# Optimization experiments

Hardware: AMD Instinct MI355X
Metric: run time of the kernel (lower is better)

The kernel has to match this reference:

```python
import jax, jax.numpy as jnp
import numpy as np

B, T, C, NH = 8, 1024, 768, 12
HD = C // NH


def setup_inputs() -> dict:
    key = jax.random.key(0)
    k1, k2, k3, k4, k5 = jax.random.split(key, 5)
    s = 0.02
    return {
        "x": jax.random.normal(k1, (B, T, C), dtype=jnp.float32),
        "w_attn": jax.random.normal(k2, (C, 3 * C), dtype=jnp.float32) * s,
        "b_attn": jax.random.normal(k3, (3 * C,), dtype=jnp.float32) * s,
        "w_proj": jax.random.normal(k4, (C, C), dtype=jnp.float32) * s,
        "b_proj": jax.random.normal(k5, (C,), dtype=jnp.float32) * s,
    }


def reference(x, w_attn, b_attn, w_proj, b_proj):
    Bv, Tv, Cv = x.shape
    # fused QKV projection
    qkv = jnp.einsum('btc,cd->btd', x, w_attn) + b_attn  # [B,T,3C]
    q, k, v = jnp.split(qkv, 3, axis=-1)
    # [B, NH, T, HD]
    q = q.reshape(Bv, Tv, NH, HD).transpose(0, 2, 1, 3)
    k = k.reshape(Bv, Tv, NH, HD).transpose(0, 2, 1, 3)
    v = v.reshape(Bv, Tv, NH, HD).transpose(0, 2, 1, 3)
    scale = 1.0 / np.sqrt(HD).astype(np.float32)
    att = jnp.einsum('bhqd,bhkd->bhqk', q, k) * scale  # [B,NH,T,T]
    causal = jnp.tril(jnp.ones((Tv, Tv), dtype=bool))
    att = jnp.where(causal, att, -jnp.inf)
    att = jax.nn.softmax(att, axis=-1)
    y = jnp.einsum('bhqk,bhkd->bhqd', att, v)  # [B,NH,T,HD]
    y = y.transpose(0, 2, 1, 3).reshape(Bv, Tv, Cv)
    return jnp.einsum('btc,cd->btd', y, w_proj) + b_proj
```

## Files before the change

kernel.cpp:

```cpp
#include <hip/hip_runtime.h>

constexpr int kB  = 8;
constexpr int kT  = 1024;
constexpr int kC  = 768;
constexpr int kNH = 12;
constexpr int kHD = 64;
constexpr int kM  = kB * kT;
constexpr int k3C = 3 * kC;

using bf16x8 = __attribute__((ext_vector_type(8))) __bf16;
using f32x4  = __attribute__((ext_vector_type(4))) float;

__device__ __forceinline__ float bf2f(unsigned short u) {
    union { unsigned int i; float f; } v;
    v.i = ((unsigned int)u) << 16;
    return v.f;
}

__device__ __forceinline__ unsigned short f2bf(float f) {
    union { float f; unsigned int u; } v; v.f = f;
    unsigned int r = v.u + 0x7fffu + ((v.u >> 16) & 1u);
    return (unsigned short)(r >> 16);
}

__device__ __forceinline__ void async16(const void* g, void* l) {
    __builtin_amdgcn_global_load_lds(
        (__attribute__((address_space(1))) void*)g,
        (__attribute__((address_space(3))) void*)l, 16, 0, 0);
}

__device__ __forceinline__ void wait_vm0() {
    __builtin_amdgcn_s_waitcnt(0x0F70);
}


__global__ __launch_bounds__(256) void cvt_bf16_kernel(
    const float* __restrict__ in, unsigned short* __restrict__ out)
{
    const int i = blockIdx.x * 256 + threadIdx.x;
    const float4 v = ((const float4*)in)[i];
    ushort4 o;
    o.x = f2bf(v.x); o.y = f2bf(v.y); o.z = f2bf(v.z); o.w = f2bf(v.w);
    ((ushort4*)out)[i] = o;
}

__global__ __launch_bounds__(256) void transpose_cvt_kernel(
    const float* __restrict__ W, unsigned short* __restrict__ Wt, int K, int N)
{
    __shared__ float tile[32][33];
    const int tx = threadIdx.x & 31, ty = threadIdx.x >> 5;
    const int n0 = blockIdx.x * 32, k0 = blockIdx.y * 32;
    #pragma unroll
    for (int i = 0; i < 4; ++i)
        tile[ty + i * 8][tx] = W[(size_t)(k0 + ty + i * 8) * N + n0 + tx];
    __syncthreads();
    #pragma unroll
    for (int i = 0; i < 4; ++i)
        Wt[(size_t)(n0 + ty + i * 8) * K + k0 + tx] = f2bf(tile[tx][ty + i * 8]);
}

__global__ __launch_bounds__(256) void vtrans_kernel(
    const unsigned short* __restrict__ qkv, unsigned short* __restrict__ VT)
{
    __shared__ unsigned short tile[64][72];
    const int tid = threadIdx.x;
    const int bh = blockIdx.x >> 4;
    const int b = bh / kNH, h = bh % kNH;
    const int tt = (blockIdx.x & 15) * 64;
    const int row = tid >> 2;
    const int c0  = (tid & 3) * 16;
    const unsigned short* src =
        qkv + (size_t)(b * kT + tt + row) * k3C + 2 * kC + h * kHD + c0;
    *(uint4*)&tile[row][c0]     = *(const uint4*)src;
    *(uint4*)&tile[row][c0 + 8] = *(const uint4*)(src + 8);
    __syncthreads();
    const int d  = tid >> 2;
    const int t8 = (tid & 3) * 16;
    unsigned short tmp[16];
    #pragma unroll
    for (int i = 0; i < 16; ++i) tmp[i] = tile[t8 + i][d];
    unsigned short* dst = VT + ((size_t)bh * kHD + d) * kT + tt + t8;
    *(uint4*)dst       = *(uint4*)&tmp[0];
    *(uint4*)(dst + 8) = *(uint4*)&tmp[8];
}

template<int NSUB, bool OUT_BF16>
__global__ __launch_bounds__(256) void gemm_mfma_kernel(
    const unsigned short* __restrict__ A, int lda,
    const unsigned short* __restrict__ Bt,
    const float* __restrict__ bias,
    void* __restrict__ outv, int N, int K)
{
    constexpr int NW = NSUB / 2;
    constexpr int BB = NSUB / 4;
    alignas(16) __shared__ unsigned short As[2][8 * 512];
    alignas(16) __shared__ unsigned short Bs[2][NSUB * 512];

    const int tid  = threadIdx.x;
    const int w    = tid >> 6;
    const int lane = tid & 63;
    const int wr = w >> 1, wc = w & 1;
    const int m0 = blockIdx.y * 128, n0 = blockIdx.x * (NSUB * 16);

    const int fr = lane & 15;
    const int fk = (lane >> 4) * 8;

    auto stage = [&](int bufi, int kt) {
        #pragma unroll
        for (int t = 0; t < 2; ++t) {
            const int fa = w * 2 + t;
            const unsigned short* ga =
                A + (size_t)(m0 + fa * 16 + fr) * lda + kt + fk;
            async16(ga, &As[bufi][fa * 512]);
        }
        #pragma unroll
        for (int t = 0; t < BB; ++t) {
            const int fb = w * BB + t;
            const unsigned short* gb =
                Bt + (size_t)(n0 + fb * 16 + fr) * K + kt + fk;
            async16(gb, &Bs[bufi][fb * 512]);
        }
    };

    f32x4 acc[4][NW];
    #pragma unroll
    for (int i = 0; i < 4; ++i)
        #pragma unroll
        for (int j = 0; j < NW; ++j) {
            f32x4 z = {0.f, 0.f, 0.f, 0.f};
            acc[i][j] = z;
        }

    stage(0, 0);
    const int niter = K / 32;
    for (int it = 0; it < niter; ++it) {
        const int buf = it & 1;
        wait_vm0();
        __syncthreads();
        if (it + 1 < niter) stage(1 - buf, (it + 1) * 32);

        bf16x8 a[4], b[NW];
        #pragma unroll
        for (int i = 0; i < 4; ++i)
            a[i] = *(const bf16x8*)&As[buf][(wr * 4 + i) * 512 + lane * 8];
        #pragma unroll
        for (int j = 0; j < NW; ++j)
            b[j] = *(const bf16x8*)&Bs[buf][(wc * NW + j) * 512 + lane * 8];
        #pragma unroll
        for (int i = 0; i < 4; ++i)
            #pragma unroll
            for (int j = 0; j < NW; ++j)
                acc[i][j] = __builtin_amdgcn_mfma_f32_16x16x32_bf16(
                    a[i], b[j], acc[i][j], 0, 0, 0);
    }

    const int quad  = lane >> 4;
    const int col16 = lane & 15;
    float biasv[NW];
    #pragma unroll
    for (int j = 0; j < NW; ++j)
        biasv[j] = bias[n0 + wc * (NW * 16) + j * 16 + col16];

    #pragma unroll
    for (int i = 0; i < 4; ++i) {
        #pragma unroll
        for (int r = 0; r < 4; ++r) {
            const int row = m0 + wr * 64 + i * 16 + quad * 4 + r;
            #pragma unroll
            for (int j = 0; j < NW; ++j) {
                const int col = n0 + wc * (NW * 16) + j * 16 + col16;
                const float v = acc[i][j][r] + biasv[j];
                if (OUT_BF16)
                    ((unsigned short*)outv)[(size_t)row * N + col] = f2bf(v);
                else
                    ((float*)outv)[(size_t)row * N + col] = v;
            }
        }
    }
}

__global__ __launch_bounds__(256) void attn_mfma_kernel(
    const unsigned short* __restrict__ qkv,
    const unsigned short* __restrict__ VT,
    unsigned short* __restrict__ y)
{
    alignas(16) __shared__ unsigned short Kf[2][8 * 512];
    alignas(16) __shared__ unsigned short Vf[2][8 * 512];
    alignas(16) __shared__ unsigned short Pf[8 * 512];

    const int tid  = threadIdx.x;
    const int w    = tid >> 6;
    const int lane = tid & 63;
    const int quad = lane >> 4, l15 = lane & 15;
    const int bh  = blockIdx.x >> 3;
    const int b   = bh / kNH, h = bh % kNH;
    const int pid = blockIdx.x & 7;

    auto stage = [&](int bufi, int kbase) {
        const unsigned short* gk = qkv +
            (size_t)(b * kT + kbase + w * 16 + l15) * k3C + kC + h * kHD + quad * 8;
        async16(gk,      &Kf[bufi][(w * 2 + 0) * 512]);
        async16(gk + 32, &Kf[bufi][(w * 2 + 1) * 512]);
        const unsigned short* gv = VT +
            ((size_t)bh * kHD + w * 16 + l15) * kT + kbase + quad * 8;
        async16(gv,      &Vf[bufi][(w * 2 + 0) * 512]);
        async16(gv + 32, &Vf[bufi][(w * 2 + 1) * 512]);
    };

    #pragma unroll 1
    for (int phase = 0; phase < 2; ++phase) {
        const int t0 = (phase == 0 ? (15 - pid) : pid) * 64;
        const int nchunks = t0 / 64 + 1;

        __syncthreads();
        stage(0, 0);
        {
            const unsigned short* g0 = qkv +
                (size_t)(b * kT + t0 + w * 16 + l15) * k3C + h * kHD + quad * 8;
            async16(g0,      &Pf[(w * 2 + 0) * 512]);
            async16(g0 + 32, &Pf[(w * 2 + 1) * 512]);
        }
        wait_vm0();
        const bf16x8 aq0 = *(const bf16x8*)&Pf[(w * 2 + 0) * 512 + lane * 8];
        const bf16x8 aq1 = *(const bf16x8*)&Pf[(w * 2 + 1) * 512 + lane * 8];

        float m_run[4], l_run[4];
        f32x4 acc_o[4];
        #pragma unroll
        for (int r = 0; r < 4; ++r) { m_run[r] = -INFINITY; l_run[r] = 0.f; }
        #pragma unroll
        for (int n = 0; n < 4; ++n) {
            f32x4 z = {0.f, 0.f, 0.f, 0.f};
            acc_o[n] = z;
        }

        for (int c = 0; c < nchunks; ++c) {
            const int kbase = c * 64;
            const int buf = c & 1;
            wait_vm0();
            __syncthreads();
            if (c + 1 < nchunks) stage(1 - buf, kbase + 64);

            f32x4 acc_s[4];
            #pragma unroll
            for (int k = 0; k < 4; ++k) {
                f32x4 z = {0.f, 0.f, 0.f, 0.f};
                acc_s[k] = z;
            }
            #pragma unroll
            for (int ksub = 0; ksub < 4; ++ksub) {
                const bf16x8 bk0 =
                    *(const bf16x8*)&Kf[buf][(ksub * 2 + 0) * 512 + lane * 8];
                const bf16x8 bk1 =
                    *(const bf16x8*)&Kf[buf][(ksub * 2 + 1) * 512 + lane * 8];
                acc_s[ksub] = __builtin_amdgcn_mfma_f32_16x16x32_bf16(
                    aq0, bk0, acc_s[ksub], 0, 0, 0);
                acc_s[ksub] = __builtin_amdgcn_mfma_f32_16x16x32_bf16(
                    aq1, bk1, acc_s[ksub], 0, 0, 0);
            }

            float sv[4][4];
            #pragma unroll
            for (int ksub = 0; ksub < 4; ++ksub)
                #pragma unroll
                for (int r = 0; r < 4; ++r)
                    sv[ksub][r] = acc_s[ksub][r] * 0.125f;
            if (kbase == t0) {
                const int qrow = t0 + w * 16 + quad * 4;
                #pragma unroll
                for (int ksub = 0; ksub < 4; ++ksub) {
                    const int key = kbase + ksub * 16 + l15;
                    #pragma unroll
                    for (int r = 0; r < 4; ++r)
                        if (key > qrow + r) sv[ksub][r] = -INFINITY;
                }
            }

            float alpha[4];
            #pragma unroll
            for (int r = 0; r < 4; ++r) {
                float mx = fmaxf(fmaxf(sv[0][r], sv[1][r]),
                                 fmaxf(sv[2][r], sv[3][r]));
                mx = fmaxf(mx, __shfl_xor(mx, 1));
                mx = fmaxf(mx, __shfl_xor(mx, 2));
                mx = fmaxf(mx, __shfl_xor(mx, 4));
                mx = fmaxf(mx, __shfl_xor(mx, 8));
                const float m_new = fmaxf(m_run[r], mx);
                alpha[r] = __expf(m_run[r] - m_new);
                float ps = 0.f;
                #pragma unroll
                for (int ksub = 0; ksub < 4; ++ksub) {
                    sv[ksub][r] = __expf(sv[ksub][r] - m_new);
                    ps += sv[ksub][r];
                }
                ps += __shfl_xor(ps, 1);
                ps += __shfl_xor(ps, 2);
                ps += __shfl_xor(ps, 4);
                ps += __shfl_xor(ps, 8);
                l_run[r] = l_run[r] * alpha[r] + ps;
                m_run[r] = m_new;
            }

            #pragma unroll
            for (int ksub = 0; ksub < 4; ++ksub) {
                const int key = ksub * 16 + l15;
                #pragma unroll
                for (int r = 0; r < 4; ++r) {
                    const int lp = quad * 4 + r + ((key & 31) >> 3) * 16;
                    Pf[(w * 2 + (key >> 5)) * 512 + lp * 8 + (key & 7)] =
                        f2bf(sv[ksub][r]);
                }
            }

            #pragma unroll
            for (int n = 0; n < 4; ++n)
                #pragma unroll
                for (int r = 0; r < 4; ++r)
                    acc_o[n][r] *= alpha[r];
            const bf16x8 ap0 = *(const bf16x8*)&Pf[(w * 2 + 0) * 512 + lane * 8];
            const bf16x8 ap1 = *(const bf16x8*)&Pf[(w * 2 + 1) * 512 + lane * 8];
            #pragma unroll
            for (int nsub = 0; nsub < 4; ++nsub) {
                const bf16x8 bv0 =
                    *(const bf16x8*)&Vf[buf][(nsub * 2 + 0) * 512 + lane * 8];
                const bf16x8 bv1 =
                    *(const bf16x8*)&Vf[buf][(nsub * 2 + 1) * 512 + lane * 8];
                acc_o[nsub] = __builtin_amdgcn_mfma_f32_16x16x32_bf16(
                    ap0, bv0, acc_o[nsub], 0, 0, 0);
                acc_o[nsub] = __builtin_amdgcn_mfma_f32_16x16x32_bf16(
                    ap1, bv1, acc_o[nsub], 0, 0, 0);
            }
        }

        float inv[4];
        #pragma unroll
        for (int r = 0; r < 4; ++r) inv[r] = 1.0f / l_run[r];
        #pragma unroll
        for (int nsub = 0; nsub < 4; ++nsub)
            #pragma unroll
            for (int r = 0; r < 4; ++r)
                y[(size_t)(b * kT + t0 + w * 16 + quad * 4 + r) * kC +
                  h * kHD + nsub * 16 + l15] = f2bf(acc_o[nsub][r] * inv[r]);
    }
}

extern "C" void kernel_launch(void* const* d_in, const int* in_sizes, int n_in,
                              void* d_out, int out_size, void* d_ws, size_t ws_size,
                              hipStream_t stream) {
    const float* x      = (const float*)d_in[0];
    const float* w_attn = (const float*)d_in[1];
    const float* b_attn = (const float*)d_in[2];
    const float* w_proj = (const float*)d_in[3];
    const float* b_proj = (const float*)d_in[4];
    float* out = (float*)d_out;

    unsigned short* xb     = (unsigned short*)d_ws;
    unsigned short* VT     = xb;
    unsigned short* wattnT = xb     + (size_t)kM * kC;
    unsigned short* wprojT = wattnT + (size_t)k3C * kC;
    unsigned short* qkv    = wprojT + (size_t)kC * kC;
    unsigned short* yb     = qkv    + (size_t)kM * k3C;

    cvt_bf16_kernel<<<(kM * kC) / (4 * 256), 256, 0, stream>>>(x, xb);
    transpose_cvt_kernel<<<dim3(k3C / 32, kC / 32), 256, 0, stream>>>(
        w_attn, wattnT, kC, k3C);
    transpose_cvt_kernel<<<dim3(kC / 32, kC / 32), 256, 0, stream>>>(
        w_proj, wprojT, kC, kC);

    gemm_mfma_kernel<8, true><<<dim3(k3C / 128, kM / 128), 256, 0, stream>>>(
        xb, kC, wattnT, b_attn, qkv, k3C, kC);

    vtrans_kernel<<<kB * kNH * (kT / 64), 256, 0, stream>>>(qkv, VT);

    attn_mfma_kernel<<<kB * kNH * 8, 256, 0, stream>>>(qkv, VT, yb);

    gemm_mfma_kernel<4, false><<<dim3(kC / 64, kM / 128), 256, 0, stream>>>(
        yb, kC, wprojT, b_proj, out, kC, kC);
}
```

Before: 242.8 us.

## Fuse V transpose into QKV GEMM epilogue and triple-buffer GEMM loads

The QKV GEMM epilogue now writes the V columns straight into the transposed per-head VT layout, using 4-element vector stores along t. Q and K go to a compact 2C-wide buffer, so the separate V-transpose kernel and its round trip through global memory are removed. The GEMM main loop moves from double to triple buffering with a partial vmcnt wait and a raw s_barrier, keeping two tiles of loads in flight. Risks are correctness of the vmcnt count against outstanding loads, and whether the raw barrier still orders LDS reads before a buffer is overwritten.

```diff
diff --git a/kernel.cpp b/kernel.cpp
--- a/kernel.cpp
+++ b/kernel.cpp
@@ -7,15 +7,10 @@
 constexpr int kHD = 64;
 constexpr int kM  = kB * kT;
 constexpr int k3C = 3 * kC;
+constexpr int kQK = 2 * kC;
 
 using bf16x8 = __attribute__((ext_vector_type(8))) __bf16;
 using f32x4  = __attribute__((ext_vector_type(4))) float;
-
-__device__ __forceinline__ float bf2f(unsigned short u) {
-    union { unsigned int i; float f; } v;
-    v.i = ((unsigned int)u) << 16;
-    return v.f;
-}
 
 __device__ __forceinline__ unsigned short f2bf(float f) {
     union { float f; unsigned int u; } v; v.f = f;
@@ -29,9 +24,10 @@
         (__attribute__((address_space(3))) void*)l, 16, 0, 0);
 }
 
-__device__ __forceinline__ void wait_vm0() {
-    __builtin_amdgcn_s_waitcnt(0x0F70);
-}
+template<int IMM> __device__ __forceinline__ void wait_vm() {
+    __builtin_amdgcn_s_waitcnt(IMM);
+}
+__device__ __forceinline__ void wait_vm0() { __builtin_amdgcn_s_waitcnt(0x0F70); }
 
 
 __global__ __launch_bounds__(256) void cvt_bf16_kernel(
@@ -59,42 +55,22 @@
         Wt[(size_t)(n0 + ty + i * 8) * K + k0 + tx] = f2bf(tile[tx][ty + i * 8]);
 }
 
-__global__ __launch_bounds__(256) void vtrans_kernel(
-    const unsigned short* __restrict__ qkv, unsigned short* __restrict__ VT)
-{
-    __shared__ unsigned short tile[64][72];
-    const int tid = threadIdx.x;
-    const int bh = blockIdx.x >> 4;
-    const int b = bh / kNH, h = bh % kNH;
-    const int tt = (blockIdx.x & 15) * 64;
-    const int row = tid >> 2;
-    const int c0  = (tid & 3) * 16;
-    const unsigned short* src =
-        qkv + (size_t)(b * kT + tt + row) * k3C + 2 * kC + h * kHD + c0;
-    *(uint4*)&tile[row][c0]     = *(const uint4*)src;
-    *(uint4*)&tile[row][c0 + 8] = *(const uint4*)(src + 8);
-    __syncthreads();
-    const int d  = tid >> 2;
-    const int t8 = (tid & 3) * 16;
-    unsigned short tmp[16];
-    #pragma unroll
-    for (int i = 0; i < 16; ++i) tmp[i] = tile[t8 + i][d];
-    unsigned short* dst = VT + ((size_t)bh * kHD + d) * kT + tt + t8;
-    *(uint4*)dst       = *(uint4*)&tmp[0];
-    *(uint4*)(dst + 8) = *(uint4*)&tmp[8];
-}
-
-template<int NSUB, bool OUT_BF16>
+template<int NSUB, int MODE>
 __global__ __launch_bounds__(256) void gemm_mfma_kernel(
     const unsigned short* __restrict__ A, int lda,
     const unsigned short* __restrict__ Bt,
     const float* __restrict__ bias,
-    void* __restrict__ outv, int N, int K)
+    void* __restrict__ outv,
+    unsigned short* __restrict__ vt,
+    int N, int K)
 {
     constexpr int NW = NSUB / 2;
-    constexpr int BB = NSUB / 4;
-    alignas(16) __shared__ unsigned short As[2][8 * 512];
-    alignas(16) __shared__ unsigned short Bs[2][NSUB * 512];
+    constexpr int BB = (NSUB / 4 > 0) ? NSUB / 4 : 1;
+    constexpr int P  = 2 + BB;
+    constexpr int WAIT_P = 0x0F70 | P;
+
+    alignas(16) __shared__ unsigned short As[3][8 * 512];
+    alignas(16) __shared__ unsigned short Bs[3][NSUB * 512];
 
     const int tid  = threadIdx.x;
     const int w    = tid >> 6;
@@ -131,27 +107,32 @@
             acc[i][j] = z;
         }
 
+    const int niter = K / 32;
     stage(0, 0);
-    const int niter = K / 32;
+    stage(1, 32);
+    int cur = 0, pf = 2;
     for (int it = 0; it < niter; ++it) {
-        const int buf = it & 1;
-        wait_vm0();
-        __syncthreads();
-        if (it + 1 < niter) stage(1 - buf, (it + 1) * 32);
+        if (it + 1 < niter) wait_vm<WAIT_P>();
+        else               wait_vm<0x0F70>();
+        __builtin_amdgcn_s_barrier();
+        if (it + 2 < niter) stage(pf, (it + 2) * 32);
 
         bf16x8 a[4], b[NW];
         #pragma unroll
         for (int i = 0; i < 4; ++i)
-            a[i] = *(const bf16x8*)&As[buf][(wr * 4 + i) * 512 + lane * 8];
+            a[i] = *(const bf16x8*)&As[cur][(wr * 4 + i) * 512 + lane * 8];
         #pragma unroll
         for (int j = 0; j < NW; ++j)
-            b[j] = *(const bf16x8*)&Bs[buf][(wc * NW + j) * 512 + lane * 8];
+            b[j] = *(const bf16x8*)&Bs[cur][(wc * NW + j) * 512 + lane * 8];
         #pragma unroll
         for (int i = 0; i < 4; ++i)
             #pragma unroll
             for (int j = 0; j < NW; ++j)
                 acc[i][j] = __builtin_amdgcn_mfma_f32_16x16x32_bf16(
                     a[i], b[j], acc[i][j], 0, 0, 0);
+
+        cur = (cur == 2) ? 0 : cur + 1;
+        pf  = (pf  == 2) ? 0 : pf  + 1;
     }
 
     const int quad  = lane >> 4;
@@ -161,26 +142,46 @@
     for (int j = 0; j < NW; ++j)
         biasv[j] = bias[n0 + wc * (NW * 16) + j * 16 + col16];
 
-    #pragma unroll
-    for (int i = 0; i < 4; ++i) {
-        #pragma unroll
-        for (int r = 0; r < 4; ++r) {
-            const int row = m0 + wr * 64 + i * 16 + quad * 4 + r;
+    if (MODE == 1 && n0 >= kQK) {
+        const int bidx = m0 >> 10;
+        #pragma unroll
+        for (int i = 0; i < 4; ++i) {
+            const int row = m0 + wr * 64 + i * 16 + quad * 4;
+            const int t = row & 1023;
             #pragma unroll
             for (int j = 0; j < NW; ++j) {
-                const int col = n0 + wc * (NW * 16) + j * 16 + col16;
-                const float v = acc[i][j][r] + biasv[j];
-                if (OUT_BF16)
-                    ((unsigned short*)outv)[(size_t)row * N + col] = f2bf(v);
-                else
-                    ((float*)outv)[(size_t)row * N + col] = v;
+                const int hv = n0 + wc * (NW * 16) + j * 16 + col16 - kQK;
+                const int h = hv >> 6, d = hv & 63;
+                ushort4 o;
+                o.x = f2bf(acc[i][j][0] + biasv[j]);
+                o.y = f2bf(acc[i][j][1] + biasv[j]);
+                o.z = f2bf(acc[i][j][2] + biasv[j]);
+                o.w = f2bf(acc[i][j][3] + biasv[j]);
+                *(ushort4*)&vt[((size_t)(bidx * kNH + h) * kHD + d) * kT + t] = o;
+            }
+        }
+    } else {
+        #pragma unroll
+        for (int i = 0; i < 4; ++i) {
+            #pragma unroll
+            for (int r = 0; r < 4; ++r) {
+                const int row = m0 + wr * 64 + i * 16 + quad * 4 + r;
+                #pragma unroll
+                for (int j = 0; j < NW; ++j) {
+                    const int col = n0 + wc * (NW * 16) + j * 16 + col16;
+                    const float v = acc[i][j][r] + biasv[j];
+                    if (MODE == 1)
+                        ((unsigned short*)outv)[(size_t)row * kQK + col] = f2bf(v);
+                    else
+                        ((float*)outv)[(size_t)row * N + col] = v;
+                }
             }
         }
     }
 }
 
 __global__ __launch_bounds__(256) void attn_mfma_kernel(
-    const unsigned short* __restrict__ qkv,
+    const unsigned short* __restrict__ qkv2,
     const unsigned short* __restrict__ VT,
     unsigned short* __restrict__ y)
 {
@@ -197,8 +198,8 @@
     const int pid = blockIdx.x & 7;
 
     auto stage = [&](int bufi, int kbase) {
-        const unsigned short* gk = qkv +
-            (size_t)(b * kT + kbase + w * 16 + l15) * k3C + kC + h * kHD + quad * 8;
+        const unsigned short* gk = qkv2 +
+            (size_t)(b * kT + kbase + w * 16 + l15) * kQK + kC + h * kHD + quad * 8;
         async16(gk,      &Kf[bufi][(w * 2 + 0) * 512]);
         async16(gk + 32, &Kf[bufi][(w * 2 + 1) * 512]);
         const unsigned short* gv = VT +
@@ -215,8 +216,8 @@
         __syncthreads();
         stage(0, 0);
         {
-            const unsigned short* g0 = qkv +
-                (size_t)(b * kT + t0 + w * 16 + l15) * k3C + h * kHD + quad * 8;
+            const unsigned short* g0 = qkv2 +
+                (size_t)(b * kT + t0 + w * 16 + l15) * kQK + h * kHD + quad * 8;
             async16(g0,      &Pf[(w * 2 + 0) * 512]);
             async16(g0 + 32, &Pf[(w * 2 + 1) * 512]);
         }
@@ -355,11 +356,11 @@
     float* out = (float*)d_out;
 
     unsigned short* xb     = (unsigned short*)d_ws;
-    unsigned short* VT     = xb;
     unsigned short* wattnT = xb     + (size_t)kM * kC;
     unsigned short* wprojT = wattnT + (size_t)k3C * kC;
-    unsigned short* qkv    = wprojT + (size_t)kC * kC;
-    unsigned short* yb     = qkv    + (size_t)kM * k3C;
+    unsigned short* qkv2   = wprojT + (size_t)kC * kC;
+    unsigned short* VT     = qkv2   + (size_t)kM * kQK;
+    unsigned short* yb     = VT     + (size_t)kNH * kB * kHD * kT;
 
     cvt_bf16_kernel<<<(kM * kC) / (4 * 256), 256, 0, stream>>>(x, xb);
     transpose_cvt_kernel<<<dim3(k3C / 32, kC / 32), 256, 0, stream>>>(
@@ -367,13 +368,11 @@
     transpose_cvt_kernel<<<dim3(kC / 32, kC / 32), 256, 0, stream>>>(
         w_proj, wprojT, kC, kC);
 
-    gemm_mfma_kernel<8, true><<<dim3(k3C / 128, kM / 128), 256, 0, stream>>>(
-        xb, kC, wattnT, b_attn, qkv, k3C, kC);
-
-    vtrans_kernel<<<kB * kNH * (kT / 64), 256, 0, stream>>>(qkv, VT);
-
-    attn_mfma_kernel<<<kB * kNH * 8, 256, 0, stream>>>(qkv, VT, yb);
-
-    gemm_mfma_kernel<4, false><<<dim3(kC / 64, kM / 128), 256, 0, stream>>>(
-        yb, kC, wprojT, b_proj, out, kC, kC);
-}
+    gemm_mfma_kernel<8, 1><<<dim3(k3C / 128, kM / 128), 256, 0, stream>>>(
+        xb, kC, wattnT, b_attn, qkv2, VT, k3C, kC);
+
+    attn_mfma_kernel<<<kB * kNH * 8, 256, 0, stream>>>(qkv2, VT, yb);
+
+    gemm_mfma_kernel<4, 0><<<dim3(kC / 64, kM / 128), 256, 0, stream>>>(
+        yb, kC, wprojT, b_proj, out, nullptr, kC, kC);
+}
```

After: 236.8 us. 1.03x faster.
